# Performance work log

Hardware: AMD Instinct MI355X
Metric: run time of the kernel (lower is better)

The kernel has to match this reference:

```python
import jax, jax.numpy as jnp
import numpy as np

B, S, D = 4, 2048, 1024

def setup_inputs() -> dict:
    key = jax.random.key(0)
    kx, kq, kk, kv = jax.random.split(key, 4)
    glorot = (6.0 / (D + D)) ** 0.5
    return {
        "x": jax.random.normal(kx, (B, S, D), dtype=jnp.float32),
        "Wq": jax.random.uniform(kq, (D, D), jnp.float32, -glorot, glorot),
        "Wk": jax.random.uniform(kk, (D, D), jnp.float32, -glorot, glorot),
        "Wv": jax.random.uniform(kv, (D, D), jnp.float32, -glorot, glorot),
    }

def reference(x, Wq, Wk, Wv):
    # q,k,v: [B,S,D]
    q = jnp.einsum("bsd,de->bse", x, Wq)
    k = jnp.einsum("bsd,de->bse", x, Wk)
    v = jnp.einsum("bsd,de->bse", x, Wv)
    scale = jnp.sqrt(jnp.asarray(q.shape[-1], q.dtype))
    scores = jnp.einsum("bqd,bkd->bqk", q, k) / scale  # [B,S,S]
    w = jax.nn.softmax(scores, axis=-1)
    return jnp.einsum("bqk,bkd->bqd", w, v)
```

## Files before the change

### kernel.cpp

```cpp
#include <hip/hip_runtime.h>
#include <hip/hip_bf16.h>


typedef _Float16 half_t;
typedef _Float16 half8 __attribute__((ext_vector_type(8)));
typedef _Float16 half4v __attribute__((ext_vector_type(4)));
typedef float f32x4 __attribute__((ext_vector_type(4)));

__device__ __forceinline__ void load16_to_lds(const half_t* g, half_t* l) {
  __builtin_amdgcn_global_load_lds(
      (const __attribute__((address_space(1))) void*)g,
      (__attribute__((address_space(3))) void*)l, 16, 0, 0);
}

#define LGKM0 asm volatile("s_waitcnt lgkmcnt(0)" ::: "memory")
#define LGKM8 asm volatile("s_waitcnt lgkmcnt(8)" ::: "memory")
#define VM4   asm volatile("s_waitcnt vmcnt(4)" ::: "memory")
#define BAR   __builtin_amdgcn_s_barrier()
#define PRIO1 __builtin_amdgcn_s_setprio(1)
#define PRIO0 __builtin_amdgcn_s_setprio(0)

__global__ __launch_bounds__(512, 2) void qkvt_gemm8(
    const half_t* __restrict__ xh, const half_t* __restrict__ wt,
    half_t* __restrict__ qk, half_t* __restrict__ vtg) {
  __shared__ __align__(16) half_t As[2][256 * 64];
  __shared__ __align__(16) half_t Bs[2][256 * 64];

  const int b = blockIdx.x;
  const half_t* A; const half_t* Bm; half_t* C;
  int ldc, m0, n0;
  if (b < 256) {
    const int x = b & 7, j = b >> 3;
    A = xh; Bm = wt; C = qk; ldc = 2048;
    m0 = (x * 4 + (j & 3)) * 256;
    n0 = (j >> 2) * 256;
  } else {
    const int idv = b - 256;
    const int x = idv & 7, j = idv >> 3;
    A = wt + (size_t)2 * 1024 * 1024; Bm = xh; C = vtg; ldc = 8192;
    m0 = (j >> 2) * 256;
    n0 = (x * 4 + (j & 3)) * 256;
  }

  const int t     = threadIdx.x;
  const int lane  = t & 63;
  const int wave  = t >> 6;
  const int wr128 = (wave >> 2) * 128;
  const int wc64  = (wave & 3) * 64;
  const int lm    = lane & 15;
  const int lq    = lane >> 4;
  const int pos0  = (lq ^ (lm & 7)) * 8;
  const int pos1  = ((4 + lq) ^ (lm & 7)) * 8;
  const int t8    = t * 8;

  const int trow = t >> 3;
  const int tchk = (t & 7) ^ (trow & 7);
  const half_t* gA0 = A  + (size_t)(m0 + trow) * 1024 + tchk * 8;
  const half_t* gB0 = Bm + (size_t)(n0 + trow) * 1024 + tchk * 8;

  f32x4 acc[8][4] = {};
  half8 va[4][2], vb0[2][2], vb1[2][2];

#define ST_A(buf, h, kt) do {                                                  \
    load16_to_lds(gA0 + (size_t)((h)*128) * 1024 + (size_t)(kt) * 64,          \
                  &As[buf][(h)*128*64] + t8);                                  \
    load16_to_lds(gA0 + (size_t)((h)*128+64) * 1024 + (size_t)(kt) * 64,       \
                  &As[buf][((h)*128+64)*64] + t8);                             \
  } while (0)
#define ST_B(buf, h, kt) do {                                                  \
    load16_to_lds(gB0 + (size_t)((h)*128) * 1024 + (size_t)(kt) * 64,          \
                  &Bs[buf][(h)*128*64] + t8);                                  \
    load16_to_lds(gB0 + (size_t)((h)*128+64) * 1024 + (size_t)(kt) * 64,       \
                  &Bs[buf][((h)*128+64)*64] + t8);                             \
  } while (0)
#define RD_A(buf, mh) do {                                                     \
    _Pragma("unroll") for (int m = 0; m < 4; ++m) {                            \
      const int ar = wr128 + (mh)*64 + m * 16 + lm;                            \
      va[m][0] = *(const half8*)&As[buf][ar * 64 + pos0];                      \
      va[m][1] = *(const half8*)&As[buf][ar * 64 + pos1];                      \
    } } while (0)
#define RD_B(buf, nh, vb) do {                                                 \
    _Pragma("unroll") for (int n = 0; n < 2; ++n) {                            \
      const int br = wc64 + (nh)*32 + n * 16 + lm;                             \
      vb[n][0] = *(const half8*)&Bs[buf][br * 64 + pos0];                      \
      vb[n][1] = *(const half8*)&Bs[buf][br * 64 + pos1];                      \
    } } while (0)
#define MF_Q(mh, nh, vb) do {                                                  \
    _Pragma("unroll") for (int kk = 0; kk < 2; ++kk)                           \
    _Pragma("unroll") for (int m = 0; m < 4; ++m)                              \
    _Pragma("unroll") for (int n = 0; n < 2; ++n)                              \
      acc[(mh)*4+m][(nh)*2+n] = __builtin_amdgcn_mfma_f32_16x16x32_f16(        \
          va[m][kk], vb[n][kk], acc[(mh)*4+m][(nh)*2+n], 0, 0, 0);             \
  } while (0)

  ST_A(0, 0, 0); ST_A(0, 1, 0);
  ST_B(0, 0, 0); ST_B(0, 1, 0);
  ST_B(1, 0, 1); ST_B(1, 1, 1);
  VM4;
  BAR;

#pragma unroll 1
  for (int i = 0; i < 8; ++i) {
    const int st1 = (2 * i + 1 < 15) ? 2 * i + 1 : 15;
    const int st2 = (2 * i + 2 < 15) ? 2 * i + 2 : 15;
    const int st3 = (2 * i + 3 < 15) ? 2 * i + 3 : 15;
    RD_A(0, 0); RD_B(0, 0, vb0);
    ST_A(1, 0, st1);
    LGKM8;
    BAR; LGKM0;
    PRIO1; MF_Q(0, 0, vb0); PRIO0;
    BAR;
    RD_B(0, 1, vb1);
    ST_A(1, 1, st1);
    BAR; LGKM0;
    PRIO1; MF_Q(0, 1, vb1); PRIO0;
    BAR;
    RD_A(0, 1);
    ST_B(0, 0, st2);
    BAR; LGKM0;
    PRIO1; MF_Q(1, 0, vb0); PRIO0;
    BAR;
    ST_B(0, 1, st2);
    BAR; LGKM0;
    PRIO1; MF_Q(1, 1, vb1); PRIO0;
    VM4;
    BAR;
    RD_A(1, 0); RD_B(1, 0, vb0);
    ST_A(0, 0, st2);
    LGKM8;
    BAR; LGKM0;
    PRIO1; MF_Q(0, 0, vb0); PRIO0;
    BAR;
    RD_B(1, 1, vb1);
    ST_A(0, 1, st2);
    BAR; LGKM0;
    PRIO1; MF_Q(0, 1, vb1); PRIO0;
    BAR;
    RD_A(1, 1);
    ST_B(1, 0, st3);
    BAR; LGKM0;
    PRIO1; MF_Q(1, 0, vb0); PRIO0;
    BAR;
    ST_B(1, 1, st3);
    BAR; LGKM0;
    PRIO1; MF_Q(1, 1, vb1); PRIO0;
    VM4;
    BAR;
  }

#pragma unroll
  for (int m = 0; m < 8; ++m)
#pragma unroll
    for (int n = 0; n < 4; ++n) {
      const int col = n0 + wc64 + n * 16 + lm;
#pragma unroll
      for (int r = 0; r < 4; ++r) {
        const int row = m0 + wr128 + m * 16 + lq * 4 + r;
        C[(size_t)row * ldc + col] = (half_t)acc[m][n][r];
      }
    }
#undef ST_A
#undef ST_B
#undef RD_A
#undef RD_B
#undef MF_Q
}

__global__ __launch_bounds__(512, 2) void scores_gemm8(
    const half_t* __restrict__ qk, half_t* __restrict__ sc,
    float* __restrict__ lpart) {
  __shared__ __align__(16) half_t As[2][256 * 64];
  __shared__ __align__(16) half_t Bs[2][256 * 64];

  const int id  = blockIdx.x;
  const int x   = id & 7, j = id >> 3;
  const int bx  = j & 7;
  const int z   = x >> 1;
  const int by  = (x & 1) * 4 + (j >> 3);
  const int m0  = by * 256;
  const int n0  = bx * 256;
  const half_t* A  = qk + (size_t)z * 2048 * 2048;
  const half_t* Bm = A + 1024;
  half_t* C = sc + (size_t)z * 2048 * 2048;

  const int t     = threadIdx.x;
  const int lane  = t & 63;
  const int wave  = t >> 6;
  const int wr128 = (wave >> 2) * 128;
  const int wc64  = (wave & 3) * 64;
  const int lm    = lane & 15;
  const int lq    = lane >> 4;
  const int pos0  = (lq ^ (lm & 7)) * 8;
  const int pos1  = ((4 + lq) ^ (lm & 7)) * 8;
  const int t8    = t * 8;

  const int trow = t >> 3;
  const int tchk = (t & 7) ^ (trow & 7);
  const half_t* gA0 = A  + (size_t)(m0 + trow) * 2048 + tchk * 8;
  const half_t* gB0 = Bm + (size_t)(n0 + trow) * 2048 + tchk * 8;

  f32x4 acc[8][4] = {};
  half8 va[4][2], vb0[2][2], vb1[2][2];

#define ST_A(buf, h, kt) do {                                                  \
    load16_to_lds(gA0 + (size_t)((h)*128) * 2048 + (size_t)(kt) * 64,          \
                  &As[buf][(h)*128*64] + t8);                                  \
    load16_to_lds(gA0 + (size_t)((h)*128+64) * 2048 + (size_t)(kt) * 64,       \
                  &As[buf][((h)*128+64)*64] + t8);                             \
  } while (0)
#define ST_B(buf, h, kt) do {                                                  \
    load16_to_lds(gB0 + (size_t)((h)*128) * 2048 + (size_t)(kt) * 64,          \
                  &Bs[buf][(h)*128*64] + t8);                                  \
    load16_to_lds(gB0 + (size_t)((h)*128+64) * 2048 + (size_t)(kt) * 64,       \
                  &Bs[buf][((h)*128+64)*64] + t8);                             \
  } while (0)
#define RD_A(buf, mh) do {                                                     \
    _Pragma("unroll") for (int m = 0; m < 4; ++m) {                            \
      const int ar = wr128 + (mh)*64 + m * 16 + lm;                            \
      va[m][0] = *(const half8*)&As[buf][ar * 64 + pos0];                      \
      va[m][1] = *(const half8*)&As[buf][ar * 64 + pos1];                      \
    } } while (0)
#define RD_B(buf, nh, vb) do {                                                 \
    _Pragma("unroll") for (int n = 0; n < 2; ++n) {                            \
      const int br = wc64 + (nh)*32 + n * 16 + lm;                             \
      vb[n][0] = *(const half8*)&Bs[buf][br * 64 + pos0];                      \
      vb[n][1] = *(const half8*)&Bs[buf][br * 64 + pos1];                      \
    } } while (0)
#define MF_Q(mh, nh, vb) do {                                                  \
    _Pragma("unroll") for (int kk = 0; kk < 2; ++kk)                           \
    _Pragma("unroll") for (int m = 0; m < 4; ++m)                              \
    _Pragma("unroll") for (int n = 0; n < 2; ++n)                              \
      acc[(mh)*4+m][(nh)*2+n] = __builtin_amdgcn_mfma_f32_16x16x32_f16(        \
          va[m][kk], vb[n][kk], acc[(mh)*4+m][(nh)*2+n], 0, 0, 0);             \
  } while (0)

  ST_A(0, 0, 0); ST_A(0, 1, 0);
  ST_B(0, 0, 0); ST_B(0, 1, 0);
  ST_B(1, 0, 1); ST_B(1, 1, 1);
  VM4;
  BAR;

#pragma unroll 1
  for (int i = 0; i < 8; ++i) {
    const int st1 = (2 * i + 1 < 15) ? 2 * i + 1 : 15;
    const int st2 = (2 * i + 2 < 15) ? 2 * i + 2 : 15;
    const int st3 = (2 * i + 3 < 15) ? 2 * i + 3 : 15;
    RD_A(0, 0); RD_B(0, 0, vb0);
    ST_A(1, 0, st1);
    LGKM8;
    BAR; LGKM0;
    PRIO1; MF_Q(0, 0, vb0); PRIO0;
    BAR;
    RD_B(0, 1, vb1);
    ST_A(1, 1, st1);
    BAR; LGKM0;
    PRIO1; MF_Q(0, 1, vb1); PRIO0;
    BAR;
    RD_A(0, 1);
    ST_B(0, 0, st2);
    BAR; LGKM0;
    PRIO1; MF_Q(1, 0, vb0); PRIO0;
    BAR;
    ST_B(0, 1, st2);
    BAR; LGKM0;
    PRIO1; MF_Q(1, 1, vb1); PRIO0;
    VM4;
    BAR;
    RD_A(1, 0); RD_B(1, 0, vb0);
    ST_A(0, 0, st2);
    LGKM8;
    BAR; LGKM0;
    PRIO1; MF_Q(0, 0, vb0); PRIO0;
    BAR;
    RD_B(1, 1, vb1);
    ST_A(0, 1, st2);
    BAR; LGKM0;
    PRIO1; MF_Q(0, 1, vb1); PRIO0;
    BAR;
    RD_A(1, 1);
    ST_B(1, 0, st3);
    BAR; LGKM0;
    PRIO1; MF_Q(1, 0, vb0); PRIO0;
    BAR;
    ST_B(1, 1, st3);
    BAR; LGKM0;
    PRIO1; MF_Q(1, 1, vb1); PRIO0;
    VM4;
    BAR;
  }

  const float scale = 1.0f / 32.0f;
#pragma unroll
  for (int m = 0; m < 8; ++m)
#pragma unroll
    for (int r = 0; r < 4; ++r) {
      const int row = m0 + wr128 + m * 16 + lq * 4 + r;
      float s = 0.f;
#pragma unroll
      for (int n = 0; n < 4; ++n) {
        const int col = n0 + wc64 + n * 16 + lm;
        float v = __expf(acc[m][n][r] * scale - 8.0f);
        s += v;
        C[(size_t)row * 2048 + col] = (half_t)v;
      }
      s += __shfl_xor(s, 1); s += __shfl_xor(s, 2);
      s += __shfl_xor(s, 4); s += __shfl_xor(s, 8);
      if (lm == 0)
        lpart[((size_t)z * 2048 + row) * 32 + bx * 4 + (wave & 3)] = s;
    }
#undef ST_A
#undef ST_B
#undef RD_A
#undef RD_B
#undef MF_Q
}

__global__ __launch_bounds__(256) void pv_gemm(
    const half_t* __restrict__ sc, const half_t* __restrict__ vtg,
    float* __restrict__ out, const float* __restrict__ lpart) {
  __shared__ __align__(16) half_t As[128 * 64];
  __shared__ __align__(16) half_t Bs[128 * 64];
  __shared__ float linv[128];

  const int z  = blockIdx.z;
  const int m0 = blockIdx.x * 128;
  const int n0 = blockIdx.y * 128;
  const half_t* A  = sc  + (size_t)z * 2048 * 2048;
  const half_t* Bm = vtg + (size_t)z * 2048;
  float* C = out + (size_t)z * 2048 * 1024;
  constexpr int lda = 2048, ldb = 8192, ldc = 1024, K = 2048;

  const int t    = threadIdx.x;
  const int wave = t >> 6;
  const int lane = t & 63;
  const int wm   = (wave >> 1) * 64;
  const int wn   = (wave & 1) * 64;
  const int lm   = lane & 15;
  const int lq   = lane >> 4;
  const int lswz = lm & 7;

  if (t < 128) {
    const float4* lp = (const float4*)&lpart[((size_t)z * 2048 + m0 + t) * 32];
    float s = 0.f;
#pragma unroll
    for (int p = 0; p < 8; ++p) {
      float4 v = lp[p];
      s += v.x + v.y + v.z + v.w;
    }
    linv[t] = 1.0f / s;
  }

  const int trow = t >> 3;
  const int tchk = (t & 7) ^ (trow & 7);

  const half_t* gA0 = A  + (size_t)(m0 + trow) * lda + tchk * 8;
  const half_t* gB0 = Bm + (size_t)(n0 + trow) * ldb + tchk * 8;
  const size_t stepA = (size_t)32 * lda;
  const size_t stepB = (size_t)32 * ldb;

  half_t* lA0 = &As[t * 8];
  half_t* lB0 = &Bs[t * 8];

  f32x4 acc[4][4] = {};

  for (int k0 = 0; k0 < K; k0 += 64) {
    __syncthreads();
#pragma unroll
    for (int n = 0; n < 4; ++n) {
      load16_to_lds(gA0 + n * stepA + k0, lA0 + n * 2048);
      load16_to_lds(gB0 + n * stepB + k0, lB0 + n * 2048);
    }
    __syncthreads();

#pragma unroll
    for (int kk = 0; kk < 2; ++kk) {
      const int pos = ((kk * 4 + lq) ^ lswz) * 8;
      half8 a[4], bf[4];
#pragma unroll
      for (int i = 0; i < 4; ++i)
        a[i] = *(const half8*)&As[(wm + i * 16 + lm) * 64 + pos];
#pragma unroll
      for (int j = 0; j < 4; ++j)
        bf[j] = *(const half8*)&Bs[(wn + j * 16 + lm) * 64 + pos];
#pragma unroll
      for (int i = 0; i < 4; ++i)
#pragma unroll
        for (int j = 0; j < 4; ++j)
          acc[i][j] = __builtin_amdgcn_mfma_f32_16x16x32_f16(a[i], bf[j], acc[i][j], 0, 0, 0);
    }
  }

#pragma unroll
  for (int i = 0; i < 4; ++i)
#pragma unroll
    for (int r = 0; r < 4; ++r) {
      const int lrow = wm + i * 16 + lq * 4 + r;
      const float inv = linv[lrow];
      const int row = m0 + lrow;
#pragma unroll
      for (int j = 0; j < 4; ++j) {
        const int col = n0 + wn + j * 16 + lm;
        C[(size_t)row * ldc + col] = acc[i][j][r] * inv;
      }
    }
}

__global__ __launch_bounds__(256) void prep(
    const float* __restrict__ x, half_t* __restrict__ xh,
    const float* __restrict__ Wq, const float* __restrict__ Wk,
    const float* __restrict__ Wv, half_t* __restrict__ wt) {
  __shared__ half_t tile[32][33];
  const int b = blockIdx.x;
  const int t = threadIdx.x;
  if (b < 8192) {
    const int i = (b * 256 + t) * 4;
    const float4 v = *reinterpret_cast<const float4*>(x + i);
    half4v o;
    o.x = (half_t)v.x; o.y = (half_t)v.y; o.z = (half_t)v.z; o.w = (half_t)v.w;
    *reinterpret_cast<half4v*>(xh + i) = o;
  } else {
    int bb = b - 8192;
    const int w = bb >> 10; bb &= 1023;
    const float* in = (w == 0) ? Wq : (w == 1) ? Wk : Wv;
    half_t* o = wt + (size_t)w * 1024 * 1024;
    const int r0 = (bb >> 5) * 32, c0 = (bb & 31) * 32;
    const int tx = t & 31, ty = t >> 5;
#pragma unroll
    for (int i = 0; i < 32; i += 8)
      tile[ty + i][tx] = (half_t)in[(size_t)(r0 + ty + i) * 1024 + c0 + tx];
    __syncthreads();
#pragma unroll
    for (int i = 0; i < 32; i += 8)
      o[(size_t)(c0 + ty + i) * 1024 + r0 + tx] = tile[tx][ty + i];
  }
}

extern "C" void kernel_launch(void* const* d_in, const int* in_sizes, int n_in,
                              void* d_out, int out_size, void* d_ws, size_t ws_size,
                              hipStream_t stream) {
  constexpr int Bb = 4, S = 2048, D = 1024;
  constexpr size_t MS = (size_t)Bb * S;

  const float* x  = (const float*)d_in[0];
  const float* Wq = (const float*)d_in[1];
  const float* Wk = (const float*)d_in[2];
  const float* Wv = (const float*)d_in[3];
  float* out = (float*)d_out;

  char* p = (char*)d_ws;
  half_t* xh    = (half_t*)p; p += MS * D * 2;
  half_t* wt    = (half_t*)p; p += (size_t)3 * D * D * 2;
  half_t* qk    = (half_t*)p; p += MS * (size_t)(2 * D) * 2;
  half_t* vtg   = (half_t*)p; p += (size_t)D * MS * 2;
  half_t* sc    = (half_t*)p; p += (size_t)Bb * S * S * 2;
  float*  lpart = (float*)p;  p += MS * 32 * 4;

  prep<<<11264, 256, 0, stream>>>(x, xh, Wq, Wk, Wv, wt);
  qkvt_gemm8<<<384, 512, 0, stream>>>(xh, wt, qk, vtg);
  scores_gemm8<<<256, 512, 0, stream>>>(qk, sc, lpart);
  pv_gemm<<<dim3(16, 8, Bb), 256, 0, stream>>>(sc, vtg, out, lpart);
}
```

Baseline: 236.5 us.

## Fuse V^T GEMM tiles into QK GEMM blocks to balance work over 256 blocks

The QKV projection previously launched 384 blocks: 256 for the Q/K tiles and 128 for the V^T tiles. Now each of 256 blocks computes its 256x256 QK tile and then a 128x256 slice of V^T, reusing the same LDS buffers. With 256 CUs this is meant to avoid a second partial wave of blocks. The cost is a longer serial tail per block and a separate smaller-tile V loop with its own pipeline prologue, which runs at lower MFMA density.

```diff
diff --git a/kernel.cpp b/kernel.cpp
--- a/kernel.cpp
+++ b/kernel.cpp
@@ -15,7 +15,9 @@
 
 #define LGKM0 asm volatile("s_waitcnt lgkmcnt(0)" ::: "memory")
 #define LGKM8 asm volatile("s_waitcnt lgkmcnt(8)" ::: "memory")
+#define VM0   asm volatile("s_waitcnt vmcnt(0)" ::: "memory")
 #define VM4   asm volatile("s_waitcnt vmcnt(4)" ::: "memory")
+#define VM6   asm volatile("s_waitcnt vmcnt(6)" ::: "memory")
 #define BAR   __builtin_amdgcn_s_barrier()
 #define PRIO1 __builtin_amdgcn_s_setprio(1)
 #define PRIO0 __builtin_amdgcn_s_setprio(0)
@@ -27,20 +29,9 @@
   __shared__ __align__(16) half_t Bs[2][256 * 64];
 
   const int b = blockIdx.x;
-  const half_t* A; const half_t* Bm; half_t* C;
-  int ldc, m0, n0;
-  if (b < 256) {
-    const int x = b & 7, j = b >> 3;
-    A = xh; Bm = wt; C = qk; ldc = 2048;
-    m0 = (x * 4 + (j & 3)) * 256;
-    n0 = (j >> 2) * 256;
-  } else {
-    const int idv = b - 256;
-    const int x = idv & 7, j = idv >> 3;
-    A = wt + (size_t)2 * 1024 * 1024; Bm = xh; C = vtg; ldc = 8192;
-    m0 = (j >> 2) * 256;
-    n0 = (x * 4 + (j & 3)) * 256;
-  }
+  const int x = b & 7, j = b >> 3;
+  const int m0 = (x * 4 + (j & 3)) * 256;
+  const int n0 = (j >> 2) * 256;
 
   const int t     = threadIdx.x;
   const int lane  = t & 63;
@@ -55,8 +46,8 @@
 
   const int trow = t >> 3;
   const int tchk = (t & 7) ^ (trow & 7);
-  const half_t* gA0 = A  + (size_t)(m0 + trow) * 1024 + tchk * 8;
-  const half_t* gB0 = Bm + (size_t)(n0 + trow) * 1024 + tchk * 8;
+  const half_t* gA0 = xh + (size_t)(m0 + trow) * 1024 + tchk * 8;
+  const half_t* gB0 = wt + (size_t)(n0 + trow) * 1024 + tchk * 8;
 
   f32x4 acc[8][4] = {};
   half8 va[4][2], vb0[2][2], vb1[2][2];
@@ -156,7 +147,7 @@
 #pragma unroll
       for (int r = 0; r < 4; ++r) {
         const int row = m0 + wr128 + m * 16 + lq * 4 + r;
-        C[(size_t)row * ldc + col] = (half_t)acc[m][n][r];
+        qk[(size_t)row * 2048 + col] = (half_t)acc[m][n][r];
       }
     }
 #undef ST_A
@@ -164,6 +155,113 @@
 #undef RD_A
 #undef RD_B
 #undef MF_Q
+
+  const int m0v = (j >> 2) * 128;
+  const int n0v = (x * 4 + (j & 3)) * 256;
+  const int wmv = (wave >> 2) * 64;
+  const int wnv = (wave & 3) * 64;
+
+  const half_t* gA2 = wt + (size_t)2 * 1024 * 1024 +
+                      (size_t)(m0v + trow) * 1024 + tchk * 8;
+  const half_t* gB2 = xh + (size_t)(n0v + trow) * 1024 + tchk * 8;
+
+  f32x4 acc2[4][4] = {};
+
+#define ST_A2(buf, kt) do {                                                    \
+    load16_to_lds(gA2 + (size_t)(kt) * 64, &As[buf][0] + t8);                  \
+    load16_to_lds(gA2 + (size_t)64 * 1024 + (size_t)(kt) * 64,                 \
+                  &As[buf][64*64] + t8);                                       \
+  } while (0)
+#define ST_B2(buf, h, kt) do {                                                 \
+    load16_to_lds(gB2 + (size_t)((h)*128) * 1024 + (size_t)(kt) * 64,          \
+                  &Bs[buf][(h)*128*64] + t8);                                  \
+    load16_to_lds(gB2 + (size_t)((h)*128+64) * 1024 + (size_t)(kt) * 64,       \
+                  &Bs[buf][((h)*128+64)*64] + t8);                             \
+  } while (0)
+#define RD_A2(buf, mh) do {                                                    \
+    _Pragma("unroll") for (int m = 0; m < 2; ++m) {                            \
+      const int ar = wmv + (mh)*32 + m * 16 + lm;                              \
+      va[(mh)*2+m][0] = *(const half8*)&As[buf][ar * 64 + pos0];               \
+      va[(mh)*2+m][1] = *(const half8*)&As[buf][ar * 64 + pos1];               \
+    } } while (0)
+#define RD_B2(buf, nh, vb) do {                                                \
+    _Pragma("unroll") for (int n = 0; n < 2; ++n) {                            \
+      const int br = wnv + (nh)*32 + n * 16 + lm;                              \
+      vb[n][0] = *(const half8*)&Bs[buf][br * 64 + pos0];                      \
+      vb[n][1] = *(const half8*)&Bs[buf][br * 64 + pos1];                      \
+    } } while (0)
+#define MF_V(mh, nh, vb) do {                                                  \
+    _Pragma("unroll") for (int kk = 0; kk < 2; ++kk)                           \
+    _Pragma("unroll") for (int m = 0; m < 2; ++m)                              \
+    _Pragma("unroll") for (int n = 0; n < 2; ++n)                              \
+      acc2[(mh)*2+m][(nh)*2+n] = __builtin_amdgcn_mfma_f32_16x16x32_f16(       \
+          va[(mh)*2+m][kk], vb[n][kk], acc2[(mh)*2+m][(nh)*2+n], 0, 0, 0);     \
+  } while (0)
+
+  VM0;
+  ST_B2(0, 0, 0); ST_B2(0, 1, 0); ST_A2(0, 0);
+  ST_B2(1, 0, 1); ST_B2(1, 1, 1); ST_A2(1, 1);
+  VM6;
+  BAR;
+
+#pragma unroll 1
+  for (int i = 0; i < 8; ++i) {
+    const int t2 = (2 * i + 2 < 15) ? 2 * i + 2 : 15;
+    const int t3 = (2 * i + 3 < 15) ? 2 * i + 3 : 15;
+    RD_A2(0, 0); RD_B2(0, 0, vb0);
+    BAR; LGKM0;
+    PRIO1; MF_V(0, 0, vb0); PRIO0;
+    BAR;
+    RD_B2(0, 1, vb1);
+    BAR; LGKM0;
+    PRIO1; MF_V(0, 1, vb1); PRIO0;
+    BAR;
+    RD_A2(0, 1);
+    ST_B2(0, 0, t2);
+    BAR; LGKM0;
+    PRIO1; MF_V(1, 0, vb0); PRIO0;
+    BAR;
+    ST_B2(0, 1, t2); ST_A2(0, t2);
+    BAR; LGKM0;
+    PRIO1; MF_V(1, 1, vb1); PRIO0;
+    VM6;
+    BAR;
+    RD_A2(1, 0); RD_B2(1, 0, vb0);
+    BAR; LGKM0;
+    PRIO1; MF_V(0, 0, vb0); PRIO0;
+    BAR;
+    RD_B2(1, 1, vb1);
+    BAR; LGKM0;
+    PRIO1; MF_V(0, 1, vb1); PRIO0;
+    BAR;
+    RD_A2(1, 1);
+    ST_B2(1, 0, t3);
+    BAR; LGKM0;
+    PRIO1; MF_V(1, 0, vb0); PRIO0;
+    BAR;
+    ST_B2(1, 1, t3); ST_A2(1, t3);
+    BAR; LGKM0;
+    PRIO1; MF_V(1, 1, vb1); PRIO0;
+    VM6;
+    BAR;
+  }
+
+#pragma unroll
+  for (int m = 0; m < 4; ++m)
+#pragma unroll
+    for (int n = 0; n < 4; ++n) {
+      const int col = n0v + wnv + n * 16 + lm;
+#pragma unroll
+      for (int r = 0; r < 4; ++r) {
+        const int row = m0v + wmv + m * 16 + lq * 4 + r;
+        vtg[(size_t)row * 8192 + col] = (half_t)acc2[m][n][r];
+      }
+    }
+#undef ST_A2
+#undef ST_B2
+#undef RD_A2
+#undef RD_B2
+#undef MF_V
 }
 
 __global__ __launch_bounds__(512, 2) void scores_gemm8(
@@ -456,7 +554,7 @@
   float*  lpart = (float*)p;  p += MS * 32 * 4;
 
   prep<<<11264, 256, 0, stream>>>(x, xh, Wq, Wk, Wv, wt);
-  qkvt_gemm8<<<384, 512, 0, stream>>>(xh, wt, qk, vtg);
+  qkvt_gemm8<<<256, 512, 0, stream>>>(xh, wt, qk, vtg);
   scores_gemm8<<<256, 512, 0, stream>>>(qk, sc, lpart);
   pv_gemm<<<dim3(16, 8, Bb), 256, 0, stream>>>(sc, vtg, out, lpart);
 }
```

After: 223.6 us. 1.06x faster.
